# Performance work log

Hardware: AMD Instinct MI355X
Metric: run time of the kernel (lower is better)

The kernel has to match this reference:

```python
import jax, jax.numpy as jnp
import numpy as np

N_USERS = 100000
N_ITEMS = 100000
D_FEAT = 256
BATCH = 8192
CLASSES = 5
E = 500000
D_CONV = 128
D_RAW = 256
D_EMB = 256
NUM_BASIS = 2
BN_EPS = 1e-3  # tf.contrib.layers.batch_norm default epsilon


def _bn_params(key, dim):
    # packed [gamma, beta, moving_mean, moving_var]
    return jnp.stack([jnp.ones(dim), jnp.zeros(dim), jnp.zeros(dim), jnp.ones(dim)]).astype(jnp.float32)


def setup_inputs() -> dict:
    key = jax.random.key(0)
    ks = jax.random.split(key, 24)
    s = lambda fan_in, fan_out: np.sqrt(2.0 / (fan_in + fan_out)).astype(np.float32)
    inp = {
        'user_feat': jax.random.normal(ks[0], (N_USERS, D_FEAT), jnp.float32),
        'item_feat': jax.random.normal(ks[1], (N_ITEMS, D_FEAT), jnp.float32),
        'user_idx': jax.random.randint(ks[2], (BATCH,), 0, N_USERS, jnp.int32),
        'item_idx': jax.random.randint(ks[3], (BATCH,), 0, N_ITEMS, jnp.int32),
        'user_edge_src': jax.random.randint(ks[4], (CLASSES, E), 0, N_ITEMS, jnp.int32),
        'user_edge_dst': jax.random.randint(ks[5], (CLASSES, E), 0, BATCH, jnp.int32),
        'user_edge_w': jax.random.uniform(ks[6], (CLASSES, E), jnp.float32),
        'item_edge_src': jax.random.randint(ks[7], (CLASSES, E), 0, N_USERS, jnp.int32),
        'item_edge_dst': jax.random.randint(ks[8], (CLASSES, E), 0, BATCH, jnp.int32),
        'item_edge_w': jax.random.uniform(ks[9], (CLASSES, E), jnp.float32),
        'W_fu': jax.random.normal(ks[10], (D_FEAT, D_RAW), jnp.float32) * s(D_FEAT, D_RAW),
        'b_fu': jnp.zeros((D_RAW,), jnp.float32),
        'W_fi': jax.random.normal(ks[11], (D_FEAT, D_RAW), jnp.float32) * s(D_FEAT, D_RAW),
        'b_fi': jnp.zeros((D_RAW,), jnp.float32),
        'W_uc': jax.random.normal(ks[12], (CLASSES, D_FEAT, D_CONV), jnp.float32) * s(D_FEAT, D_CONV),
        'W_ic': jax.random.normal(ks[13], (CLASSES, D_FEAT, D_CONV), jnp.float32) * s(D_FEAT, D_CONV),
        'bn_fu': _bn_params(ks[14], D_RAW),
        'bn_hu': _bn_params(ks[15], CLASSES * D_CONV),
        'bn_fi': _bn_params(ks[16], D_RAW),
        'bn_hi': _bn_params(ks[17], CLASSES * D_CONV),
        'W2_fu': jax.random.normal(ks[18], (D_RAW, D_EMB), jnp.float32) * s(D_RAW, D_EMB),
        'W2_hu': jax.random.normal(ks[19], (CLASSES * D_CONV, D_EMB), jnp.float32) * s(CLASSES * D_CONV, D_EMB),
        'W2_fi': jax.random.normal(ks[20], (D_RAW, D_EMB), jnp.float32) * s(D_RAW, D_EMB),
        'W2_hi': jax.random.normal(ks[21], (CLASSES * D_CONV, D_EMB), jnp.float32) * s(CLASSES * D_CONV, D_EMB),
        'Wdec': jax.random.normal(ks[22], (NUM_BASIS, D_EMB, D_EMB), jnp.float32) * s(D_EMB, D_EMB),
        'Wcomb': jax.random.normal(ks[23], (CLASSES, NUM_BASIS), jnp.float32) * s(CLASSES, NUM_BASIS),
    }
    return inp


def _bn(x, p):
    gamma, beta, mean, var = p[0], p[1], p[2], p[3]
    return gamma * (x - mean) * jax.lax.rsqrt(var + BN_EPS) + beta


def _agg(feat, src, dst, w, n_rows):
    # weighted sparse [B, N] x dense [N, D] aggregation via gather + segment_sum
    msgs = feat[src] * w[:, None]  # [E, D]
    return jax.ops.segment_sum(msgs, dst, num_segments=n_rows)


def reference(user_feat, item_feat, user_idx, item_idx,
              user_edge_src, user_edge_dst, user_edge_w,
              item_edge_src, item_edge_dst, item_edge_w,
              W_fu, b_fu, W_fi, b_fi, W_uc, W_ic,
              bn_fu, bn_hu, bn_fi, bn_hi,
              W2_fu, W2_hu, W2_fi, W2_hi, Wdec, Wcomb):
    B = user_idx.shape[0]
    classes = W_uc.shape[0]

    # batch row selection (sparse.matmul with one-hot selector == gather)
    f_user = user_feat[user_idx] @ W_fu + b_fu  # [B, D_RAW]
    f_item = item_feat[item_idx] @ W_fi + b_fi

    # per-class graph convolution: aggregate opposite-side features, project, stack
    h_user = jnp.concatenate(
        [_agg(item_feat, user_edge_src[c], user_edge_dst[c], user_edge_w[c], B) @ W_uc[c]
         for c in range(classes)], axis=1)  # [B, classes*D_CONV]
    h_item = jnp.concatenate(
        [_agg(user_feat, item_edge_src[c], item_edge_dst[c], item_edge_w[c], B) @ W_ic[c]
         for c in range(classes)], axis=1)

    # batchnorm (inference stats) + relu  (dropout rate 0 -> identity)
    f_user = jax.nn.relu(_bn(f_user, bn_fu))
    f_item = jax.nn.relu(_bn(f_item, bn_fi))
    h_user = jax.nn.relu(_bn(h_user, bn_hu))
    h_item = jax.nn.relu(_bn(h_item, bn_hi))

    user_emb = jax.nn.relu(f_user @ W2_fu + h_user @ W2_hu)  # [B, D_EMB]
    item_emb = jax.nn.relu(f_item @ W2_fi + h_item @ W2_hi)

    # bilinear decoder: per-class kernel = sum_k Wcomb[r,k] * Wdec[k]
    kernels = jnp.einsum('rk,kij->rij', Wcomb, Wdec)  # [classes, D_EMB, D_EMB]
    logits = jnp.einsum('bi,rij,bj->br', user_emb, kernels, item_emb)  # [B, classes]
    return logits


if __name__ == '__main__':
    out = reference(**setup_inputs())
    print(out.shape, out.dtype)
```

## Files before the change

kernel.cpp:

```cpp
#include <hip/hip_runtime.h>
#include <cstdint>
#include <cstddef>

#define NBATCH   8192
#define DFEAT    256
#define DCONV    128
#define NCLASS   5
#define NEDGE    500000
#define NUSERS   100000
#define BN_EPS   1e-3f
#define NBUCKET  128
#define BROWS    64
#define CAP      4608
#define NPH      8

typedef unsigned short u16;
typedef short bf16x8_t __attribute__((ext_vector_type(8)));
typedef float f32x4_t  __attribute__((ext_vector_type(4)));

__device__ __forceinline__ u16 f2bf(float x) {
    unsigned u = __float_as_uint(x);
    u += 0x7FFF + ((u >> 16) & 1);
    return (u16)(u >> 16);
}
__device__ __forceinline__ float bf2f(u16 h) {
    return __uint_as_float(((unsigned)h) << 16);
}

__device__ __forceinline__ void mfma_tiles(
    const u16* __restrict__ A, int lda, const int* __restrict__ gather,
    const u16* __restrict__ BT, int K,
    int tileM, int tileN, u16* As, u16* Bs, f32x4_t acc[4])
{
    const int t    = threadIdx.x;
    const int rowi = t >> 2;
    const int kc   = t & 3;
    const int w    = t >> 6;
    const int lane = t & 63;

    int ar = gather ? gather[tileM + rowi] : (tileM + rowi);
    const u16* Ap = A  + (size_t)ar * lda + kc * 8;
    const u16* Bp = BT + (size_t)(tileN + rowi) * K + kc * 8;
    u16* Aw = As + (size_t)(((rowi >> 4) * 64) + (rowi & 15) + 16 * kc) * 8;
    u16* Bw = Bs + (size_t)(((rowi >> 4) * 64) + (rowi & 15) + 16 * kc) * 8;
    const u16* Ar = As + (size_t)(w * 64 + lane) * 8;

    for (int k0 = 0; k0 < K; k0 += 32) {
        __syncthreads();
        *(uint4*)Aw = *(const uint4*)(Ap + k0);
        *(uint4*)Bw = *(const uint4*)(Bp + k0);
        __syncthreads();
        bf16x8_t av = *(const bf16x8_t*)Ar;
        #pragma unroll
        for (int nb = 0; nb < 4; ++nb) {
            bf16x8_t bv = *(const bf16x8_t*)(Bs + (size_t)(nb * 64 + lane) * 8);
            acc[nb] = __builtin_amdgcn_mfma_f32_16x16x32_bf16(av, bv, acc[nb], 0, 0, 0);
        }
    }
}

__device__ __forceinline__ void epilogue(
    f32x4_t acc[4], int tileM, int tileN,
    const float* __restrict__ bias, const float* __restrict__ bn, int bn_ld,
    int relu, u16* __restrict__ out_bf, float* __restrict__ out_f32, int ldc)
{
    const int t = threadIdx.x, w = t >> 6, lane = t & 63;
    const int row0 = tileM + w * 16 + (lane >> 4) * 4;
    #pragma unroll
    for (int nb = 0; nb < 4; ++nb) {
        int col = tileN + nb * 16 + (lane & 15);
        float g = 1.f, be = 0.f, mu = 0.f, va = 1.f, bs = 0.f;
        if (bn)   { g = bn[col]; be = bn[bn_ld + col]; mu = bn[2 * bn_ld + col]; va = bn[3 * bn_ld + col]; }
        if (bias) bs = bias[col];
        #pragma unroll
        for (int r = 0; r < 4; ++r) {
            float x = acc[nb][r] + bs;
            if (bn)   x = g * (x - mu) * rsqrtf(va + BN_EPS) + be;
            if (relu) x = fmaxf(x, 0.f);
            size_t o = (size_t)(row0 + r) * ldc + col;
            if (out_bf) out_bf[o] = f2bf(x);
            else        out_f32[o] = x;
        }
    }
}

__global__ __launch_bounds__(256) void k_gemm_f(
    const u16* __restrict__ ubf, const u16* __restrict__ ibf,
    const int* __restrict__ uidx, const int* __restrict__ iidx,
    const u16* __restrict__ WTu, const u16* __restrict__ WTi,
    const float* __restrict__ bu, const float* __restrict__ bi,
    const float* __restrict__ bnu, const float* __restrict__ bni,
    u16* __restrict__ outu, u16* __restrict__ outi)
{
    __shared__ __align__(16) u16 As[2048], Bs[2048];
    f32x4_t z4 = {0.f, 0.f, 0.f, 0.f};
    f32x4_t acc[4] = {z4, z4, z4, z4};
    int z = blockIdx.z;
    const u16* feat = z ? ibf : ubf;
    const int* idx  = z ? iidx : uidx;
    const u16* WT   = z ? WTi : WTu;
    const float* bias = z ? bi : bu;
    const float* bn   = z ? bni : bnu;
    u16* out = z ? outi : outu;
    int tileM = blockIdx.x * 64, tileN = blockIdx.y * 64;
    mfma_tiles(feat, 256, idx, WT, 256, tileM, tileN, As, Bs, acc);
    epilogue(acc, tileM, tileN, bias, bn, 256, 1, out, nullptr, 256);
}

__global__ __launch_bounds__(256) void k_hproj(
    const u16* __restrict__ agg, const u16* __restrict__ WucT, const u16* __restrict__ WicT,
    const float* __restrict__ bn_hu, const float* __restrict__ bn_hi,
    u16* __restrict__ h_user, u16* __restrict__ h_item)
{
    __shared__ __align__(16) u16 As[2048], Bs[2048];
    f32x4_t z4 = {0.f, 0.f, 0.f, 0.f};
    f32x4_t acc[4] = {z4, z4, z4, z4};
    int cs = blockIdx.z, c = cs % NCLASS, side = cs / NCLASS;
    const u16* A  = agg + (size_t)cs * NBATCH * DFEAT;
    const u16* BT = (side ? WicT : WucT) + (size_t)c * DCONV * DFEAT;
    const float* bn = (side ? bn_hi : bn_hu) + c * DCONV;
    u16* out = (side ? h_item : h_user) + c * DCONV;
    int tileM = blockIdx.x * 64, tileN = blockIdx.y * 64;
    mfma_tiles(A, 256, nullptr, BT, 256, tileM, tileN, As, Bs, acc);
    epilogue(acc, tileM, tileN, nullptr, bn, NCLASS * DCONV, 1, out, nullptr, NCLASS * DCONV);
}

__global__ __launch_bounds__(256) void k_emb(
    const u16* __restrict__ fu, const u16* __restrict__ fi,
    const u16* __restrict__ hu, const u16* __restrict__ hi,
    const u16* __restrict__ W2fTu, const u16* __restrict__ W2hTu,
    const u16* __restrict__ W2fTi, const u16* __restrict__ W2hTi,
    u16* __restrict__ embu, u16* __restrict__ embi)
{
    __shared__ __align__(16) u16 As[2048], Bs[2048];
    f32x4_t z4 = {0.f, 0.f, 0.f, 0.f};
    f32x4_t acc[4] = {z4, z4, z4, z4};
    int z = blockIdx.z;
    const u16* fbf  = z ? fi : fu;
    const u16* hbf  = z ? hi : hu;
    const u16* W2fT = z ? W2fTi : W2fTu;
    const u16* W2hT = z ? W2hTi : W2hTu;
    u16* emb = z ? embi : embu;
    int tileM = blockIdx.x * 64, tileN = blockIdx.y * 64;
    mfma_tiles(fbf, 256, nullptr, W2fT, 256, tileM, tileN, As, Bs, acc);
    mfma_tiles(hbf, NCLASS * DCONV, nullptr, W2hT, NCLASS * DCONV, tileM, tileN, As, Bs, acc);
    epilogue(acc, tileM, tileN, nullptr, nullptr, 0, 1, emb, nullptr, 256);
}

__global__ __launch_bounds__(256) void k_dec(
    const u16* __restrict__ emb, const u16* __restrict__ WdecT,
    float* __restrict__ t0, float* __restrict__ t1)
{
    __shared__ __align__(16) u16 As[2048], Bs[2048];
    f32x4_t z4 = {0.f, 0.f, 0.f, 0.f};
    f32x4_t acc[4] = {z4, z4, z4, z4};
    int zi = blockIdx.z;
    const u16* BT = WdecT + (size_t)zi * 256 * 256;
    float* out = zi ? t1 : t0;
    int tileM = blockIdx.x * 64, tileN = blockIdx.y * 64;
    mfma_tiles(emb, 256, nullptr, BT, 256, tileM, tileN, As, Bs, acc);
    epilogue(acc, tileM, tileN, nullptr, nullptr, 0, 0, nullptr, out, 256);
}

__global__ __launch_bounds__(256) void cvt_feat(
    const float* __restrict__ uf, const float* __restrict__ itf,
    u16* __restrict__ ubf, u16* __restrict__ ibf)
{
    const size_t n4 = (size_t)NUSERS * DFEAT / 4;
    for (size_t i = (size_t)blockIdx.x * 256 + threadIdx.x; i < 2 * n4;
         i += (size_t)gridDim.x * 256) {
        bool u = i < n4;
        size_t j = u ? i : i - n4;
        float4 v = u ? ((const float4*)uf)[j] : ((const float4*)itf)[j];
        ushort4 o;
        o.x = f2bf(v.x); o.y = f2bf(v.y); o.z = f2bf(v.z); o.w = f2bf(v.w);
        ((ushort4*)(u ? ubf : ibf))[j] = o;
    }
}

#define OFF_WFU   0
#define OFF_WFI   65536
#define OFF_WUC   131072
#define OFF_WIC   294912
#define OFF_W2FU  458752
#define OFF_W2HU  524288
#define OFF_W2FI  688128
#define OFF_W2HI  753664
#define OFF_WDEC  917504

__global__ __launch_bounds__(256) void cvt_wt(
    const float* __restrict__ Wfu, const float* __restrict__ Wfi,
    const float* __restrict__ Wuc, const float* __restrict__ Wic,
    const float* __restrict__ W2fu, const float* __restrict__ W2hu,
    const float* __restrict__ W2fi, const float* __restrict__ W2hi,
    const float* __restrict__ Wdec, u16* __restrict__ wT)
{
    const float* in; u16* out; int K, N, B;
    switch (blockIdx.y) {
        case 0: in = Wfu;  out = wT + OFF_WFU;  K = 256; N = 256; B = 1; break;
        case 1: in = Wfi;  out = wT + OFF_WFI;  K = 256; N = 256; B = 1; break;
        case 2: in = Wuc;  out = wT + OFF_WUC;  K = 256; N = 128; B = 5; break;
        case 3: in = Wic;  out = wT + OFF_WIC;  K = 256; N = 128; B = 5; break;
        case 4: in = W2fu; out = wT + OFF_W2FU; K = 256; N = 256; B = 1; break;
        case 5: in = W2hu; out = wT + OFF_W2HU; K = 640; N = 256; B = 1; break;
        case 6: in = W2fi; out = wT + OFF_W2FI; K = 256; N = 256; B = 1; break;
        case 7: in = W2hi; out = wT + OFF_W2HI; K = 640; N = 256; B = 1; break;
        default: in = Wdec; out = wT + OFF_WDEC; K = 256; N = 256; B = 2; break;
    }
    int total = B * K * N;
    for (int idx = blockIdx.x * 256 + threadIdx.x; idx < total; idx += gridDim.x * 256) {
        int b = idx / (K * N);
        int r = idx - b * K * N;
        int n = r / K;
        int k = r - n * K;
        out[idx] = f2bf(in[(size_t)(b * K + k) * N + n]);
    }
}

__global__ __launch_bounds__(256) void init_bcur(int* __restrict__ bcur)
{
    int i = blockIdx.x * 256 + threadIdx.x;
    if (i < 10 * NBUCKET) bcur[i] = (i & (NBUCKET - 1)) * CAP;
}

__global__ __launch_bounds__(256) void partition_kernel(
    const int* __restrict__ u_src, const int* __restrict__ u_dst, const float* __restrict__ u_w,
    const int* __restrict__ i_src, const int* __restrict__ i_dst, const float* __restrict__ i_w,
    int* __restrict__ bcur, uint2* __restrict__ part)
{
    __shared__ int hist[NBUCKET];
    __shared__ int cur[NBUCKET];
    int cs = blockIdx.y;
    const int* srcp; const int* dstp; const float* wp;
    if (cs < NCLASS) {
        srcp = u_src + (size_t)cs * NEDGE;
        dstp = u_dst + (size_t)cs * NEDGE;
        wp   = u_w   + (size_t)cs * NEDGE;
    } else {
        int c = cs - NCLASS;
        srcp = i_src + (size_t)c * NEDGE;
        dstp = i_dst + (size_t)c * NEDGE;
        wp   = i_w   + (size_t)c * NEDGE;
    }
    int lo_e = (int)(((long long)blockIdx.x * NEDGE) / gridDim.x);
    int hi_e = (int)(((long long)(blockIdx.x + 1) * NEDGE) / gridDim.x);

    for (int i = threadIdx.x; i < NBUCKET; i += 256) hist[i] = 0;
    __syncthreads();
    for (int e = lo_e + threadIdx.x; e < hi_e; e += 256)
        atomicAdd(&hist[dstp[e] >> 6], 1);
    __syncthreads();
    for (int i = threadIdx.x; i < NBUCKET; i += 256)
        cur[i] = atomicAdd(&bcur[cs * NBUCKET + i], hist[i]);
    __syncthreads();
    uint2* out = part + (size_t)cs * NBUCKET * CAP;
    for (int e = lo_e + threadIdx.x; e < hi_e; e += 256) {
        int dst = dstp[e];
        int bkt = dst >> 6;
        int pos = atomicAdd(&cur[bkt], 1);
        if (pos < bkt * CAP + CAP)
            out[pos] = make_uint2((unsigned)srcp[e] | ((unsigned)(dst & 63) << 24),
                                  __float_as_uint(wp[e]));
    }
}

__device__ __forceinline__ int edge_key(unsigned x) {
    return (int)((x >> 24) * NPH) + (int)(((x & 0xFFFFFF) >> 14) & (NPH - 1));
}

__global__ __launch_bounds__(512) void spmm_sorted(
    const u16* __restrict__ item_bf, const u16* __restrict__ user_bf,
    const uint2* __restrict__ part, const int* __restrict__ bcur,
    u16* __restrict__ agg)
{
    __shared__ int bin_cnt[BROWS * NPH];
    __shared__ int bin_off[BROWS * NPH + 1];
    __shared__ int bin_cur[BROWS * NPH];
    __shared__ int wsum[8];
    __shared__ __align__(8) uint2 sorted[CAP];
    int b  = blockIdx.x;
    int cs = blockIdx.y;
    const u16* feat = (cs < NCLASS) ? item_bf : user_bf;
    int n = bcur[cs * NBUCKET + b] - b * CAP;
    if (n > CAP) n = CAP;
    const uint2* ew = part + ((size_t)cs * NBUCKET + b) * CAP;
    int tid = threadIdx.x, wave = tid >> 6, lane = tid & 63;

    bin_cnt[tid] = 0;
    __syncthreads();
    for (int e = tid; e < n; e += 512)
        atomicAdd(&bin_cnt[edge_key(ew[e].x)], 1);
    __syncthreads();
    {
        int c = bin_cnt[tid];
        int v = c;
        #pragma unroll
        for (int o = 1; o < 64; o <<= 1) {
            int u = __shfl_up(v, o);
            if (lane >= o) v += u;
        }
        if (lane == 63) wsum[wave] = v;
        __syncthreads();
        if (tid < 8) {
            int s = wsum[tid];
            #pragma unroll
            for (int o = 1; o < 8; o <<= 1) {
                int u = __shfl_up(s, o);
                if (lane >= o) s += u;
            }
            wsum[tid] = s;
        }
        __syncthreads();
        int base = wave ? wsum[wave - 1] : 0;
        int incl = v + base;
        bin_off[tid + 1] = incl;
        bin_cur[tid] = incl - c;
        if (tid == 0) bin_off[0] = 0;
    }
    __syncthreads();
    for (int e = tid; e < n; e += 512) {
        uint2 p = ew[e];
        int pos = atomicAdd(&bin_cur[edge_key(p.x)], 1);
        sorted[pos] = p;
    }
    __syncthreads();

    int rowbase = cs * NBATCH + b * BROWS;
    float ax[8], ay[8], az[8], aw[8];
    #pragma unroll
    for (int r0 = 0; r0 < 8; ++r0) { ax[r0] = 0.f; ay[r0] = 0.f; az[r0] = 0.f; aw[r0] = 0.f; }

    for (int ph = 0; ph < NPH; ++ph) {
        #pragma unroll
        for (int r0 = 0; r0 < 8; ++r0) {
            int bi = (wave * 8 + r0) * NPH + ph;
            int j0 = bin_off[bi], j1 = bin_off[bi + 1];
            int j = j0;
            for (; j + 7 < j1; j += 8) {
                uint2 p[8];
                #pragma unroll
                for (int q = 0; q < 8; ++q) p[q] = sorted[j + q];
                ushort4 v[8];
                #pragma unroll
                for (int q = 0; q < 8; ++q)
                    v[q] = *(const ushort4*)&feat[(size_t)(p[q].x & 0xFFFFFF) * DFEAT + lane * 4];
                #pragma unroll
                for (int q = 0; q < 8; ++q) {
                    float w = __uint_as_float(p[q].y);
                    ax[r0] += w * bf2f(v[q].x);
                    ay[r0] += w * bf2f(v[q].y);
                    az[r0] += w * bf2f(v[q].z);
                    aw[r0] += w * bf2f(v[q].w);
                }
            }
            for (; j + 3 < j1; j += 4) {
                uint2 p0 = sorted[j], p1 = sorted[j + 1], p2 = sorted[j + 2], p3 = sorted[j + 3];
                ushort4 v0 = *(const ushort4*)&feat[(size_t)(p0.x & 0xFFFFFF) * DFEAT + lane * 4];
                ushort4 v1 = *(const ushort4*)&feat[(size_t)(p1.x & 0xFFFFFF) * DFEAT + lane * 4];
                ushort4 v2 = *(const ushort4*)&feat[(size_t)(p2.x & 0xFFFFFF) * DFEAT + lane * 4];
                ushort4 v3 = *(const ushort4*)&feat[(size_t)(p3.x & 0xFFFFFF) * DFEAT + lane * 4];
                float w0 = __uint_as_float(p0.y), w1 = __uint_as_float(p1.y);
                float w2 = __uint_as_float(p2.y), w3 = __uint_as_float(p3.y);
                ax[r0] += w0 * bf2f(v0.x) + w1 * bf2f(v1.x) + w2 * bf2f(v2.x) + w3 * bf2f(v3.x);
                ay[r0] += w0 * bf2f(v0.y) + w1 * bf2f(v1.y) + w2 * bf2f(v2.y) + w3 * bf2f(v3.y);
                az[r0] += w0 * bf2f(v0.z) + w1 * bf2f(v1.z) + w2 * bf2f(v2.z) + w3 * bf2f(v3.z);
                aw[r0] += w0 * bf2f(v0.w) + w1 * bf2f(v1.w) + w2 * bf2f(v2.w) + w3 * bf2f(v3.w);
            }
            for (; j < j1; ++j) {
                uint2 p0 = sorted[j];
                ushort4 v0 = *(const ushort4*)&feat[(size_t)(p0.x & 0xFFFFFF) * DFEAT + lane * 4];
                float w0 = __uint_as_float(p0.y);
                ax[r0] += w0 * bf2f(v0.x);
                ay[r0] += w0 * bf2f(v0.y);
                az[r0] += w0 * bf2f(v0.z);
                aw[r0] += w0 * bf2f(v0.w);
            }
        }
    }

    #pragma unroll
    for (int r0 = 0; r0 < 8; ++r0) {
        ushort4 o4;
        o4.x = f2bf(ax[r0]); o4.y = f2bf(ay[r0]); o4.z = f2bf(az[r0]); o4.w = f2bf(aw[r0]);
        *(ushort4*)&agg[(size_t)(rowbase + wave * 8 + r0) * 256 + lane * 4] = o4;
    }
}

__global__ __launch_bounds__(256) void decoder_kernel(
    const float* __restrict__ t0, const float* __restrict__ t1,
    const u16* __restrict__ item_emb, const float* __restrict__ Wcomb,
    float* __restrict__ out)
{
    int wave = threadIdx.x >> 6;
    int lane = threadIdx.x & 63;
    int b = blockIdx.x * 4 + wave;
    const u16*   ie = item_emb + (size_t)b * 256;
    const float* p0 = t0 + (size_t)b * 256;
    const float* p1 = t1 + (size_t)b * 256;
    float s0 = 0.f, s1 = 0.f;
    #pragma unroll
    for (int j = lane; j < 256; j += 64) {
        float v = bf2f(ie[j]);
        s0 += p0[j] * v;
        s1 += p1[j] * v;
    }
    #pragma unroll
    for (int o = 32; o > 0; o >>= 1) {
        s0 += __shfl_down(s0, o);
        s1 += __shfl_down(s1, o);
    }
    if (lane == 0) {
        #pragma unroll
        for (int r = 0; r < NCLASS; ++r)
            out[b * NCLASS + r] = Wcomb[r * 2 + 0] * s0 + Wcomb[r * 2 + 1] * s1;
    }
}

extern "C" void kernel_launch(void* const* d_in, const int* in_sizes, int n_in,
                              void* d_out, int out_size, void* d_ws, size_t ws_size,
                              hipStream_t stream)
{
    const float* user_feat = (const float*)d_in[0];
    const float* item_feat = (const float*)d_in[1];
    const int*   user_idx  = (const int*)  d_in[2];
    const int*   item_idx  = (const int*)  d_in[3];
    const int*   u_src     = (const int*)  d_in[4];
    const int*   u_dst     = (const int*)  d_in[5];
    const float* u_w       = (const float*)d_in[6];
    const int*   i_src     = (const int*)  d_in[7];
    const int*   i_dst     = (const int*)  d_in[8];
    const float* i_w       = (const float*)d_in[9];
    const float* W_fu      = (const float*)d_in[10];
    const float* b_fu      = (const float*)d_in[11];
    const float* W_fi      = (const float*)d_in[12];
    const float* b_fi      = (const float*)d_in[13];
    const float* W_uc      = (const float*)d_in[14];
    const float* W_ic      = (const float*)d_in[15];
    const float* bn_fu     = (const float*)d_in[16];
    const float* bn_hu     = (const float*)d_in[17];
    const float* bn_fi     = (const float*)d_in[18];
    const float* bn_hi     = (const float*)d_in[19];
    const float* W2_fu     = (const float*)d_in[20];
    const float* W2_hu     = (const float*)d_in[21];
    const float* W2_fi     = (const float*)d_in[22];
    const float* W2_hi     = (const float*)d_in[23];
    const float* Wdec      = (const float*)d_in[24];
    const float* Wcomb     = (const float*)d_in[25];
    float* out = (float*)d_out;

    char* ws = (char*)d_ws;
    int*   bcur       = (int*)  (ws + 0);
    uint2* part_ew    = (uint2*)(ws + 65536);
    u16*   user_bf    = (u16*)  (ws + 47251456);
    u16*   item_bf    = (u16*)  (ws + 98451456);
    u16*   agg_bf     = (u16*)  (ws + 149651456);
    u16*   wT         = (u16*)  (ws + 191594496);
    u16*   f_user_bf  = (u16*)  (ws + 65536);
    u16*   f_item_bf  = (u16*)  (ws + 4259840);
    u16*   h_user_bf  = (u16*)  (ws + 8454144);
    u16*   h_item_bf  = (u16*)  (ws + 18939904);
    float* t0         = (float*)(ws + 149651456);
    float* t1         = (float*)(ws + 158040064);
    u16*   user_emb   = (u16*)  (ws + 166428672);
    u16*   item_emb   = (u16*)  (ws + 170622976);

    init_bcur<<<5, 256, 0, stream>>>(bcur);
    partition_kernel<<<dim3(128, 10), 256, 0, stream>>>(
        u_src, u_dst, u_w, i_src, i_dst, i_w, bcur, part_ew);

    cvt_feat<<<4096, 256, 0, stream>>>(user_feat, item_feat, user_bf, item_bf);
    cvt_wt<<<dim3(160, 9), 256, 0, stream>>>(W_fu, W_fi, W_uc, W_ic,
                                             W2_fu, W2_hu, W2_fi, W2_hi, Wdec, wT);

    spmm_sorted<<<dim3(NBUCKET, 10), 512, 0, stream>>>(
        item_bf, user_bf, part_ew, bcur, agg_bf);

    k_gemm_f<<<dim3(128, 4, 2), 256, 0, stream>>>(
        user_bf, item_bf, user_idx, item_idx, wT + OFF_WFU, wT + OFF_WFI,
        b_fu, b_fi, bn_fu, bn_fi, f_user_bf, f_item_bf);

    k_hproj<<<dim3(128, 2, 10), 256, 0, stream>>>(agg_bf, wT + OFF_WUC, wT + OFF_WIC,
                                                  bn_hu, bn_hi, h_user_bf, h_item_bf);

    k_emb<<<dim3(128, 4, 2), 256, 0, stream>>>(
        f_user_bf, f_item_bf, h_user_bf, h_item_bf,
        wT + OFF_W2FU, wT + OFF_W2HU, wT + OFF_W2FI, wT + OFF_W2HI,
        user_emb, item_emb);

    k_dec<<<dim3(128, 4, 2), 256, 0, stream>>>(user_emb, wT + OFF_WDEC, t0, t1);
    decoder_kernel<<<NBATCH / 4, 256, 0, stream>>>(t0, t1, item_emb, Wcomb, out);
}
```

Baseline: 739.7 us.

## Finer source binning in SpMM, interleave sides, tiled weight transpose, fp32 gather GEMM

The SpMM bins edges by finer source ranges (8K-row slices, 13 bins used out of 16 slots) to improve cache locality of feature gathers. Its grid is flattened so user and item sides interleave across blocks. The weight conversion kernel becomes an LDS-tiled transpose with coalesced reads and writes. The feature GEMM now reads fp32 features directly and converts them in-kernel, which adds more global traffic for that GEMM. The edge_key shift relies on node indices staying below 13*8192.

```diff
diff --git a/kernel.cpp b/kernel.cpp
--- a/kernel.cpp
+++ b/kernel.cpp
@@ -12,7 +12,8 @@
 #define NBUCKET  128
 #define BROWS    64
 #define CAP      4608
-#define NPH      8
+#define NPHB     16
+#define NPHU     13
 
 typedef unsigned short u16;
 typedef short bf16x8_t __attribute__((ext_vector_type(8)));
@@ -27,8 +28,9 @@
     return __uint_as_float(((unsigned)h) << 16);
 }
 
-__device__ __forceinline__ void mfma_tiles(
-    const u16* __restrict__ A, int lda, const int* __restrict__ gather,
+template<int AF32>
+__device__ __forceinline__ void mfma_tiles_t(
+    const void* __restrict__ Av, int lda, const int* __restrict__ gather,
     const u16* __restrict__ BT, int K,
     int tileM, int tileN, u16* As, u16* Bs, f32x4_t acc[4])
 {
@@ -39,7 +41,8 @@
     const int lane = t & 63;
 
     int ar = gather ? gather[tileM + rowi] : (tileM + rowi);
-    const u16* Ap = A  + (size_t)ar * lda + kc * 8;
+    const u16*   Ap16 = (const u16*)Av   + (size_t)ar * lda + kc * 8;
+    const float* Apf  = (const float*)Av + (size_t)ar * lda + kc * 8;
     const u16* Bp = BT + (size_t)(tileN + rowi) * K + kc * 8;
     u16* Aw = As + (size_t)(((rowi >> 4) * 64) + (rowi & 15) + 16 * kc) * 8;
     u16* Bw = Bs + (size_t)(((rowi >> 4) * 64) + (rowi & 15) + 16 * kc) * 8;
@@ -47,7 +50,17 @@
 
     for (int k0 = 0; k0 < K; k0 += 32) {
         __syncthreads();
-        *(uint4*)Aw = *(const uint4*)(Ap + k0);
+        if (AF32) {
+            float4 a0 = *(const float4*)(Apf + k0);
+            float4 a1 = *(const float4*)(Apf + k0 + 4);
+            ushort4 p0, p1;
+            p0.x = f2bf(a0.x); p0.y = f2bf(a0.y); p0.z = f2bf(a0.z); p0.w = f2bf(a0.w);
+            p1.x = f2bf(a1.x); p1.y = f2bf(a1.y); p1.z = f2bf(a1.z); p1.w = f2bf(a1.w);
+            *(ushort4*)Aw = p0;
+            *(ushort4*)(Aw + 4) = p1;
+        } else {
+            *(uint4*)Aw = *(const uint4*)(Ap16 + k0);
+        }
         *(uint4*)Bw = *(const uint4*)(Bp + k0);
         __syncthreads();
         bf16x8_t av = *(const bf16x8_t*)Ar;
@@ -85,7 +98,7 @@
 }
 
 __global__ __launch_bounds__(256) void k_gemm_f(
-    const u16* __restrict__ ubf, const u16* __restrict__ ibf,
+    const float* __restrict__ uf, const float* __restrict__ itf,
     const int* __restrict__ uidx, const int* __restrict__ iidx,
     const u16* __restrict__ WTu, const u16* __restrict__ WTi,
     const float* __restrict__ bu, const float* __restrict__ bi,
@@ -96,14 +109,14 @@
     f32x4_t z4 = {0.f, 0.f, 0.f, 0.f};
     f32x4_t acc[4] = {z4, z4, z4, z4};
     int z = blockIdx.z;
-    const u16* feat = z ? ibf : ubf;
+    const float* feat = z ? itf : uf;
     const int* idx  = z ? iidx : uidx;
     const u16* WT   = z ? WTi : WTu;
     const float* bias = z ? bi : bu;
     const float* bn   = z ? bni : bnu;
     u16* out = z ? outi : outu;
     int tileM = blockIdx.x * 64, tileN = blockIdx.y * 64;
-    mfma_tiles(feat, 256, idx, WT, 256, tileM, tileN, As, Bs, acc);
+    mfma_tiles_t<1>(feat, 256, idx, WT, 256, tileM, tileN, As, Bs, acc);
     epilogue(acc, tileM, tileN, bias, bn, 256, 1, out, nullptr, 256);
 }
 
@@ -121,7 +134,7 @@
     const float* bn = (side ? bn_hi : bn_hu) + c * DCONV;
     u16* out = (side ? h_item : h_user) + c * DCONV;
     int tileM = blockIdx.x * 64, tileN = blockIdx.y * 64;
-    mfma_tiles(A, 256, nullptr, BT, 256, tileM, tileN, As, Bs, acc);
+    mfma_tiles_t<0>(A, 256, nullptr, BT, 256, tileM, tileN, As, Bs, acc);
     epilogue(acc, tileM, tileN, nullptr, bn, NCLASS * DCONV, 1, out, nullptr, NCLASS * DCONV);
 }
 
@@ -142,8 +155,8 @@
     const u16* W2hT = z ? W2hTi : W2hTu;
     u16* emb = z ? embi : embu;
     int tileM = blockIdx.x * 64, tileN = blockIdx.y * 64;
-    mfma_tiles(fbf, 256, nullptr, W2fT, 256, tileM, tileN, As, Bs, acc);
-    mfma_tiles(hbf, NCLASS * DCONV, nullptr, W2hT, NCLASS * DCONV, tileM, tileN, As, Bs, acc);
+    mfma_tiles_t<0>(fbf, 256, nullptr, W2fT, 256, tileM, tileN, As, Bs, acc);
+    mfma_tiles_t<0>(hbf, NCLASS * DCONV, nullptr, W2hT, NCLASS * DCONV, tileM, tileN, As, Bs, acc);
     epilogue(acc, tileM, tileN, nullptr, nullptr, 0, 1, emb, nullptr, 256);
 }
 
@@ -158,7 +171,7 @@
     const u16* BT = WdecT + (size_t)zi * 256 * 256;
     float* out = zi ? t1 : t0;
     int tileM = blockIdx.x * 64, tileN = blockIdx.y * 64;
-    mfma_tiles(emb, 256, nullptr, BT, 256, tileM, tileN, As, Bs, acc);
+    mfma_tiles_t<0>(emb, 256, nullptr, BT, 256, tileM, tileN, As, Bs, acc);
     epilogue(acc, tileM, tileN, nullptr, nullptr, 0, 0, nullptr, out, 256);
 }
 
@@ -195,6 +208,7 @@
     const float* __restrict__ W2fi, const float* __restrict__ W2hi,
     const float* __restrict__ Wdec, u16* __restrict__ wT)
 {
+    __shared__ float tile[32][33];
     const float* in; u16* out; int K, N, B;
     switch (blockIdx.y) {
         case 0: in = Wfu;  out = wT + OFF_WFU;  K = 256; N = 256; B = 1; break;
@@ -207,13 +221,26 @@
         case 7: in = W2hi; out = wT + OFF_W2HI; K = 640; N = 256; B = 1; break;
         default: in = Wdec; out = wT + OFF_WDEC; K = 256; N = 256; B = 2; break;
     }
-    int total = B * K * N;
-    for (int idx = blockIdx.x * 256 + threadIdx.x; idx < total; idx += gridDim.x * 256) {
-        int b = idx / (K * N);
-        int r = idx - b * K * N;
-        int n = r / K;
-        int k = r - n * K;
-        out[idx] = f2bf(in[(size_t)(b * K + k) * N + n]);
+    int tk = K >> 5, tn = N >> 5;
+    int tid = blockIdx.x;
+    if (tid >= B * tk * tn) return;
+    int b  = tid / (tk * tn);
+    int r  = tid - b * tk * tn;
+    int kt = r % tk, nt = r / tk;
+    int k0 = kt * 32, n0 = nt * 32;
+    int ty = threadIdx.x >> 5, tx = threadIdx.x & 31;
+    const float* ip = in + (size_t)b * K * N;
+    u16* op = out + (size_t)b * N * K;
+    #pragma unroll
+    for (int i = 0; i < 4; ++i) {
+        int row = ty + 8 * i;
+        tile[row][tx] = ip[(size_t)(k0 + row) * N + (n0 + tx)];
+    }
+    __syncthreads();
+    #pragma unroll
+    for (int i = 0; i < 4; ++i) {
+        int row = ty + 8 * i;
+        op[(size_t)(n0 + row) * K + (k0 + tx)] = f2bf(tile[tx][row]);
     }
 }
 
@@ -265,7 +292,7 @@
 }
 
 __device__ __forceinline__ int edge_key(unsigned x) {
-    return (int)((x >> 24) * NPH) + (int)(((x & 0xFFFFFF) >> 14) & (NPH - 1));
+    return (int)((x >> 24) * NPHB) + (int)((x & 0xFFFFFFu) >> 13);
 }
 
 __global__ __launch_bounds__(512) void spmm_sorted(
@@ -273,27 +300,34 @@
     const uint2* __restrict__ part, const int* __restrict__ bcur,
     u16* __restrict__ agg)
 {
-    __shared__ int bin_cnt[BROWS * NPH];
-    __shared__ int bin_off[BROWS * NPH + 1];
-    __shared__ int bin_cur[BROWS * NPH];
+    __shared__ int bin_cnt[BROWS * NPHB];
+    __shared__ int bin_off[BROWS * NPHB + 1];
+    __shared__ int bin_cur[BROWS * NPHB];
     __shared__ int wsum[8];
     __shared__ __align__(8) uint2 sorted[CAP];
-    int b  = blockIdx.x;
-    int cs = blockIdx.y;
-    const u16* feat = (cs < NCLASS) ? item_bf : user_bf;
+    int id   = blockIdx.x;
+    int side = id & 1;
+    int k    = id >> 1;
+    int c    = k >> 7;
+    int b    = k & 127;
+    int cs   = side * NCLASS + c;
+    const u16* feat = side ? user_bf : item_bf;
     int n = bcur[cs * NBUCKET + b] - b * CAP;
     if (n > CAP) n = CAP;
     const uint2* ew = part + ((size_t)cs * NBUCKET + b) * CAP;
     int tid = threadIdx.x, wave = tid >> 6, lane = tid & 63;
 
     bin_cnt[tid] = 0;
+    bin_cnt[tid + 512] = 0;
     __syncthreads();
     for (int e = tid; e < n; e += 512)
         atomicAdd(&bin_cnt[edge_key(ew[e].x)], 1);
     __syncthreads();
     {
-        int c = bin_cnt[tid];
-        int v = c;
+        int i2 = tid * 2;
+        int c0 = bin_cnt[i2], c1 = bin_cnt[i2 + 1];
+        int s = c0 + c1;
+        int v = s;
         #pragma unroll
         for (int o = 1; o < 64; o <<= 1) {
             int u = __shfl_up(v, o);
@@ -302,20 +336,21 @@
         if (lane == 63) wsum[wave] = v;
         __syncthreads();
         if (tid < 8) {
-            int s = wsum[tid];
+            int s8 = wsum[tid];
             #pragma unroll
             for (int o = 1; o < 8; o <<= 1) {
-                int u = __shfl_up(s, o);
-                if (lane >= o) s += u;
+                int u = __shfl_up(s8, o);
+                if (lane >= o) s8 += u;
             }
-            wsum[tid] = s;
+            wsum[tid] = s8;
         }
         __syncthreads();
-        int base = wave ? wsum[wave - 1] : 0;
-        int incl = v + base;
-        bin_off[tid + 1] = incl;
-        bin_cur[tid] = incl - c;
-        if (tid == 0) bin_off[0] = 0;
+        int base = (wave ? wsum[wave - 1] : 0) + (v - s);
+        bin_off[i2] = base;
+        bin_off[i2 + 1] = base + c0;
+        bin_cur[i2] = base;
+        bin_cur[i2 + 1] = base + c0;
+        if (tid == 511) bin_off[1024] = base + s;
     }
     __syncthreads();
     for (int e = tid; e < n; e += 512) {
@@ -330,10 +365,10 @@
     #pragma unroll
     for (int r0 = 0; r0 < 8; ++r0) { ax[r0] = 0.f; ay[r0] = 0.f; az[r0] = 0.f; aw[r0] = 0.f; }
 
-    for (int ph = 0; ph < NPH; ++ph) {
+    for (int ph = 0; ph < NPHU; ++ph) {
         #pragma unroll
         for (int r0 = 0; r0 < 8; ++r0) {
-            int bi = (wave * 8 + r0) * NPH + ph;
+            int bi = (wave * 8 + r0) * NPHB + ph;
             int j0 = bin_off[bi], j1 = bin_off[bi + 1];
             int j = j0;
             for (; j + 7 < j1; j += 8) {
@@ -472,11 +507,11 @@
     cvt_wt<<<dim3(160, 9), 256, 0, stream>>>(W_fu, W_fi, W_uc, W_ic,
                                              W2_fu, W2_hu, W2_fi, W2_hi, Wdec, wT);
 
-    spmm_sorted<<<dim3(NBUCKET, 10), 512, 0, stream>>>(
+    spmm_sorted<<<dim3(2 * NCLASS * NBUCKET), 512, 0, stream>>>(
         item_bf, user_bf, part_ew, bcur, agg_bf);
 
     k_gemm_f<<<dim3(128, 4, 2), 256, 0, stream>>>(
-        user_bf, item_bf, user_idx, item_idx, wT + OFF_WFU, wT + OFF_WFI,
+        user_feat, item_feat, user_idx, item_idx, wT + OFF_WFU, wT + OFF_WFI,
         b_fu, b_fi, bn_fu, bn_fi, f_user_bf, f_item_bf);
 
     k_hproj<<<dim3(128, 2, 10), 256, 0, stream>>>(agg_bf, wT + OFF_WUC, wT + OFF_WIC,
```

Measured after the change: 710.2 us. -4.0%, faster.
